# Kernel tuning notes

Measured on AMD Instinct MI355X. Metric: run time of the kernel, lower is better.

The kernel has to match this reference:

```python
import jax, jax.numpy as jnp
import numpy as np

CHANNELS = 8
IN_CHANNELS = 8
MASK_OUT_STRIDE = 4
WEIGHT_NUMS = [(IN_CHANNELS + 2) * CHANNELS, CHANNELS * CHANNELS, CHANNELS * 1]
BIAS_NUMS = [CHANNELS, CHANNELS, 1]
SOI = jnp.array([8.0, 16.0, 32.0, 64.0, 128.0], dtype=jnp.float32)
EPS = 1e-5


def compute_locations(h, w, stride):
    # (x, y) center of each stride-sized cell, row-major (y outer, x inner)
    sx = jnp.arange(w, dtype=jnp.float32) * stride + stride // 2
    sy = jnp.arange(h, dtype=jnp.float32) * stride + stride // 2
    yy, xx = jnp.meshgrid(sy, sx, indexing='ij')
    return jnp.stack([xx.reshape(-1), yy.reshape(-1)], axis=-1)  # [H*W, 2]


def aligned_bilinear(t, factor):
    # Matches AdelaiDet aligned_bilinear: replicate-pad right/bottom, bilinear
    # upsample align_corners=True to (f*h+1, f*w+1), replicate-pad top/left by
    # f//2, crop to (f*h, f*w).
    if factor == 1:
        return t
    n, c, h, w = t.shape
    t = jnp.pad(t, ((0, 0), (0, 0), (0, 1), (0, 1)), mode='edge')  # [n,c,h+1,w+1]
    oh, ow = factor * h + 1, factor * w + 1
    ys = jnp.arange(oh, dtype=jnp.float32) / factor  # align_corners mapping
    xs = jnp.arange(ow, dtype=jnp.float32) / factor
    y0 = jnp.floor(ys).astype(jnp.int32)
    x0 = jnp.floor(xs).astype(jnp.int32)
    y1 = jnp.minimum(y0 + 1, h)
    x1 = jnp.minimum(x0 + 1, w)
    wy = (ys - y0.astype(jnp.float32)).astype(t.dtype)
    wx = (xs - x0.astype(jnp.float32)).astype(t.dtype)
    ty = t[:, :, y0, :] * (1.0 - wy)[None, None, :, None] + t[:, :, y1, :] * wy[None, None, :, None]
    out = ty[:, :, :, x0] * (1.0 - wx) + ty[:, :, :, x1] * wx
    p = factor // 2
    out = jnp.pad(out, ((0, 0), (0, 0), (p, 0), (p, 0)), mode='edge')
    return out[:, :, :oh - 1, :ow - 1]


def parse_dynamic_params(params):
    n = params.shape[0]
    splits = jnp.split(params, np.cumsum(WEIGHT_NUMS + BIAS_NUMS)[:-1], axis=1)
    w0 = splits[0].reshape(n, CHANNELS, IN_CHANNELS + 2)
    w1 = splits[1].reshape(n, CHANNELS, CHANNELS)
    w2 = splits[2].reshape(n, 1, CHANNELS)
    b0 = splits[3].reshape(n, CHANNELS)
    b1 = splits[4].reshape(n, CHANNELS)
    b2 = splits[5].reshape(n, 1)
    return (w0, w1, w2), (b0, b1, b2)


def setup_inputs() -> dict:
    key = jax.random.key(0)
    ks = jax.random.split(key, 6)
    N, H, W = 2, 100, 136
    n_inst = 500
    return {
        'mask_feats': jax.random.normal(ks[0], (N, IN_CHANNELS, H, W), dtype=jnp.float32),
        'mask_head_params': jax.random.normal(ks[1], (n_inst, 169), dtype=jnp.float32),
        'locations_inst': jax.random.uniform(ks[2], (n_inst, 2), dtype=jnp.float32),
        'gt_bitmasks': jax.random.uniform(ks[3], (n_inst, 1, 2 * H, 2 * W), dtype=jnp.float32),
        'im_inds': jax.random.randint(ks[4], (n_inst,), 0, N, dtype=jnp.int64 if jax.config.jax_enable_x64 else jnp.int32),
        'fpn_levels': jax.random.randint(ks[5], (n_inst,), 0, 5, dtype=jnp.int64 if jax.config.jax_enable_x64 else jnp.int32),
        'mask_feat_stride': 8,
    }


def reference(mask_feats, mask_head_params, locations_inst, gt_bitmasks, im_inds, fpn_levels, mask_feat_stride):
    N, Cin, H, W = mask_feats.shape
    n = mask_head_params.shape[0]
    # relative coordinates, normalized by per-instance size-of-interest
    locs = compute_locations(H, W, mask_feat_stride)                 # [HW, 2]
    rel = locations_inst[:, None, :] - locs[None, :, :]              # [n, HW, 2]
    rel = jnp.transpose(rel, (0, 2, 1))                              # [n, 2, HW]
    soi = SOI[fpn_levels]                                            # [n]
    rel = (rel / soi[:, None, None]).astype(mask_feats.dtype)
    feats = mask_feats[im_inds].reshape(n, Cin, H * W)               # gather per instance
    x = jnp.concatenate([rel, feats], axis=1)                        # [n, Cin+2, HW]
    # per-instance 1x1 conv stack == batched small GEMMs
    (w0, w1, w2), (b0, b1, b2) = parse_dynamic_params(mask_head_params)
    x = jax.nn.relu(jnp.einsum('nci,nip->ncp', w0, x) + b0[:, :, None])
    x = jax.nn.relu(jnp.einsum('nci,nip->ncp', w1, x) + b1[:, :, None])
    x = jnp.einsum('nci,nip->ncp', w2, x) + b2[:, :, None]           # [n, 1, HW]
    logits = x.reshape(n, 1, H, W)
    logits = aligned_bilinear(logits, mask_feat_stride // MASK_OUT_STRIDE)
    scores = jax.nn.sigmoid(logits)                                  # [n, 1, 2H, 2W]
    # dice loss
    xs = scores.reshape(n, -1)
    t = gt_bitmasks.reshape(n, -1)
    inter = jnp.sum(xs * t, axis=1)
    union = jnp.sum(xs * xs, axis=1) + jnp.sum(t * t, axis=1) + EPS
    loss = 1.0 - 2.0 * inter / union
    return jnp.mean(loss)
```

## Files before the change

kernel.cpp:

```cpp
#include <hip/hip_runtime.h>
#include <hip/hip_bf16.h>
#include <math.h>

#define CIN      8
#define H_IN     100
#define W_IN     136
#define NPIX     (H_IN * W_IN)
#define OH       (2 * H_IN)
#define OW       (2 * W_IN)
#define ONPIX    (OH * OW)
#define NPARAMS  169
#define EPSV     1e-5f
#define NSLICE   4
#define KG4      34
#define KGROUPS  34
#define TASKS_B  (25 * KGROUPS)


__device__ __forceinline__ float sigmoidf_fast(float x) {
    float e = __expf(-x);
    return __builtin_amdgcn_rcpf(1.f + e);
}

__global__ __launch_bounds__(256, 4)
void mask_head_fused(const float* __restrict__ mask_feats,
                     const float* __restrict__ params,
                     const float* __restrict__ locs,
                     const float* __restrict__ gt,
                     const int*   __restrict__ im_inds,
                     const int*   __restrict__ fpn_levels,
                     float*       __restrict__ partials)
{
    const int inst  = blockIdx.x >> 2;
    const int slice = blockIdx.x & 3;
    const int tid   = threadIdx.x;

    const int r_start = (slice == 0) ? 0 : 25 * slice - 1;
    const int nrows   = (slice == 0) ? 25 : 26;
    const int ntask   = nrows * KG4;

    __shared__ float s_logit[26 * W_IN];
    __shared__ float s_red[12];

    const float* __restrict__ wp = params + (size_t)inst * NPARAMS;

    const int   im  = im_inds[inst];
    const int   lvl = fpn_levels[inst];
    const float inv_soi = exp2f(-(float)(3 + lvl));
    const float lx = locs[inst * 2 + 0];
    const float ly = locs[inst * 2 + 1];
    const float dx8 = 8.f * inv_soi;

    const float* feat = mask_feats + (size_t)im * (CIN * NPIX);
    const int goff = r_start * W_IN;

    #pragma unroll 1
    for (int it = 0; it < 4; ++it) {
        const int t = it * 256 + tid;
        const bool valid = t < ntask;
        const int tc = valid ? t : ntask - 1;
        const int r  = tc / KG4;
        const int k  = tc - r * KG4;
        const int lpx = r * W_IN + 4 * k;
        const float* fb = feat + (goff + lpx);

        float4 f[8];
        #pragma unroll
        for (int c = 0; c < CIN; ++c)
            f[c] = *(const float4*)(fb + c * NPIX);

        float in0[4];
        in0[0] = (lx - (float)(32 * k + 4)) * inv_soi;
        in0[1] = in0[0] - dx8;
        in0[2] = in0[1] - dx8;
        in0[3] = in0[2] - dx8;
        const float in1 = (ly - (float)((r_start + r) * 8 + 4)) * inv_soi;

        float o4[4];

#define DO_PX(J, COMP)                                                        \
        {                                                                     \
            float aj[8];                                                      \
            _Pragma("unroll")                                                 \
            for (int o = 0; o < 8; ++o)                                       \
                aj[o] = fmaf(wp[o * 10], in0[J],                              \
                             fmaf(wp[o * 10 + 1], in1, wp[152 + o]));         \
            _Pragma("unroll")                                                 \
            for (int c = 0; c < 8; ++c) {                                     \
                _Pragma("unroll")                                             \
                for (int o = 0; o < 8; ++o)                                   \
                    aj[o] = fmaf(wp[o * 10 + 2 + c], f[c].COMP, aj[o]);       \
            }                                                                 \
            _Pragma("unroll")                                                 \
            for (int o = 0; o < 8; ++o)                                       \
                aj[o] = fmaxf(aj[o], 0.f);                                    \
            float acc = wp[168];                                              \
            _Pragma("unroll")                                                 \
            for (int o = 0; o < 8; ++o) {                                     \
                float tt = wp[160 + o];                                       \
                _Pragma("unroll")                                             \
                for (int i = 0; i < 8; ++i)                                   \
                    tt = fmaf(wp[80 + o * 8 + i], aj[i], tt);                 \
                acc = fmaf(wp[144 + o], fmaxf(tt, 0.f), acc);                 \
            }                                                                 \
            o4[J] = acc;                                                      \
        }

        DO_PX(0, x)
        DO_PX(1, y)
        DO_PX(2, z)
        DO_PX(3, w)
#undef DO_PX

        if (valid) {
            float4 ov = {o4[0], o4[1], o4[2], o4[3]};
            *(float4*)(s_logit + lpx) = ov;
        }
    }

    __syncthreads();

    float inter = 0.f, ssum = 0.f, tsum = 0.f;
    const float* gtp = gt + (size_t)inst * ONPIX;
    const int pair_base = 25 * slice;

    #pragma unroll 1
    for (int base = 0; base < TASKS_B; base += 256) {
        const int task = base + tid;
        if (task < TASKS_B) {
            const int pl = task / KGROUPS;
            const int k  = task - pl * KGROUPS;
            const int pg = pair_base + pl;
            const int er = pg - r_start;
            const int pr = (pg > 0 ? pg - 1 : 0) - r_start;
            const float* E = s_logit + er * W_IN;
            const float* P = s_logit + pr * W_IN;
            const int c0  = 4 * k;
            const int cm1 = (k > 0) ? c0 - 1 : 0;

            const float* g0 = gtp + (size_t)(2 * pg) * OW + 8 * k;
            const float4 ga = *(const float4*)(g0);
            const float4 gb = *(const float4*)(g0 + 4);
            const float4 gc = *(const float4*)(g0 + OW);
            const float4 gd = *(const float4*)(g0 + OW + 4);
            const float4 e4 = *(const float4*)(E + c0);
            const float  em = E[cm1];
            const float4 p4 = *(const float4*)(P + c0);
            const float  pm = P[cm1];

            const float ecur[4] = {e4.x, e4.y, e4.z, e4.w};
            const float pcur[4] = {p4.x, p4.y, p4.z, p4.w};
            const float gav[8] = {ga.x, ga.y, ga.z, ga.w, gb.x, gb.y, gb.z, gb.w};
            const float gex[8] = {gc.x, gc.y, gc.z, gc.w, gd.x, gd.y, gd.z, gd.w};

            float Se_prev = em;
            float Sa_prev = 0.5f * (em + pm);
            #pragma unroll
            for (int j = 0; j < 4; ++j) {
                const float Se = ecur[j];
                const float Sa = 0.5f * (ecur[j] + pcur[j]);
                {
                    float s = sigmoidf_fast(0.5f * (Sa_prev + Sa));
                    float t2 = gav[2 * j];
                    inter = fmaf(s, t2, inter); ssum = fmaf(s, s, ssum); tsum = fmaf(t2, t2, tsum);
                    s = sigmoidf_fast(Sa);
                    t2 = gav[2 * j + 1];
                    inter = fmaf(s, t2, inter); ssum = fmaf(s, s, ssum); tsum = fmaf(t2, t2, tsum);
                }
                {
                    float s = sigmoidf_fast(0.5f * (Se_prev + Se));
                    float t2 = gex[2 * j];
                    inter = fmaf(s, t2, inter); ssum = fmaf(s, s, ssum); tsum = fmaf(t2, t2, tsum);
                    s = sigmoidf_fast(Se);
                    t2 = gex[2 * j + 1];
                    inter = fmaf(s, t2, inter); ssum = fmaf(s, s, ssum); tsum = fmaf(t2, t2, tsum);
                }
                Se_prev = Se;
                Sa_prev = Sa;
            }
        }
    }

    #pragma unroll
    for (int off = 32; off > 0; off >>= 1) {
        inter += __shfl_down(inter, off, 64);
        ssum  += __shfl_down(ssum,  off, 64);
        tsum  += __shfl_down(tsum,  off, 64);
    }
    const int wid = tid >> 6;
    if ((tid & 63) == 0) {
        s_red[wid * 3 + 0] = inter;
        s_red[wid * 3 + 1] = ssum;
        s_red[wid * 3 + 2] = tsum;
    }
    __syncthreads();
    if (tid == 0) {
        float I = 0.f, S = 0.f, T = 0.f;
        #pragma unroll
        for (int w = 0; w < 4; ++w) {
            I += s_red[w * 3 + 0];
            S += s_red[w * 3 + 1];
            T += s_red[w * 3 + 2];
        }
        partials[blockIdx.x * 3 + 0] = I;
        partials[blockIdx.x * 3 + 1] = S;
        partials[blockIdx.x * 3 + 2] = T;
    }
}

__global__ __launch_bounds__(512)
void loss_mean_kernel(const float* __restrict__ partials, float* __restrict__ out, int n)
{
    __shared__ float s_red[8];
    float v = 0.f;
    for (int i = threadIdx.x; i < n; i += 512) {
        float I = 0.f, S = 0.f, T = 0.f;
        #pragma unroll
        for (int s = 0; s < NSLICE; ++s) {
            const float* p = partials + (size_t)(i * NSLICE + s) * 3;
            I += p[0];
            S += p[1];
            T += p[2];
        }
        v += 1.f - 2.f * I / (S + T + EPSV);
    }
    #pragma unroll
    for (int off = 32; off > 0; off >>= 1) v += __shfl_down(v, off, 64);
    const int wid = threadIdx.x >> 6;
    if ((threadIdx.x & 63) == 0) s_red[wid] = v;
    __syncthreads();
    if (threadIdx.x == 0) {
        float s = 0.f;
        #pragma unroll
        for (int w = 0; w < 8; ++w) s += s_red[w];
        out[0] = s / (float)n;
    }
}

extern "C" void kernel_launch(void* const* d_in, const int* in_sizes, int n_in,
                              void* d_out, int out_size, void* d_ws, size_t ws_size,
                              hipStream_t stream)
{
    const float* mask_feats = (const float*)d_in[0];
    const float* params     = (const float*)d_in[1];
    const float* locs       = (const float*)d_in[2];
    const float* gt         = (const float*)d_in[3];
    const int*   im_inds    = (const int*)d_in[4];
    const int*   fpn_levels = (const int*)d_in[5];

    const int n = in_sizes[4];
    float* partials = (float*)d_ws;

    mask_head_fused<<<n * NSLICE, 256, 0, stream>>>(mask_feats, params, locs, gt,
                                                    im_inds, fpn_levels, partials);
    loss_mean_kernel<<<1, 512, 0, stream>>>(partials, (float*)d_out, n);
}
```

Before: 182.4 us.

## Prefetch first ground-truth rows into LDS asynchronously during conv phase

In the first iteration of the per-pixel conv loop, each block issues asynchronous global-to-LDS loads covering the first 11 row-pairs of its slice of the ground-truth mask. The later dice pass then reads those rows from LDS and fetches the rest from global memory as before. The aim is to hide part of the ground-truth fetch latency behind the conv arithmetic. The cost is about 24KB more LDS per block, which may lower occupancy, and the LDS prefetch is issued only by threads that have a valid conv task in the first iteration.

```diff
diff --git a/kernel.cpp b/kernel.cpp
--- a/kernel.cpp
+++ b/kernel.cpp
@@ -1,5 +1,4 @@
 #include <hip/hip_runtime.h>
-#include <hip/hip_bf16.h>
 #include <math.h>
 
 #define CIN      8
@@ -16,6 +15,13 @@
 #define KGROUPS  34
 #define TASKS_B  (25 * KGROUPS)
 
+#define GT_PRE_PAIRS 11
+#define GT_PRE_ROWS  (2 * GT_PRE_PAIRS)
+#define GT_PRE_F4    (GT_PRE_ROWS * OW / 4)
+
+#define GLOBAL_AS __attribute__((address_space(1)))
+#define LDS_AS    __attribute__((address_space(3)))
+
 
 __device__ __forceinline__ float sigmoidf_fast(float x) {
     float e = __expf(-x);
@@ -40,6 +46,7 @@
     const int ntask   = nrows * KG4;
 
     __shared__ float s_logit[26 * W_IN];
+    __shared__ float s_gt[GT_PRE_ROWS * OW];
     __shared__ float s_red[12];
 
     const float* __restrict__ wp = params + (size_t)inst * NPARAMS;
@@ -54,65 +61,80 @@
     const float* feat = mask_feats + (size_t)im * (CIN * NPIX);
     const int goff = r_start * W_IN;
 
+    const float* gtp  = gt + (size_t)inst * ONPIX;
+    const float* gpre = gtp + (size_t)(50 * slice) * OW;
+
     #pragma unroll 1
     for (int it = 0; it < 4; ++it) {
         const int t = it * 256 + tid;
-        const bool valid = t < ntask;
-        const int tc = valid ? t : ntask - 1;
-        const int r  = tc / KG4;
-        const int k  = tc - r * KG4;
-        const int lpx = r * W_IN + 4 * k;
-        const float* fb = feat + (goff + lpx);
-
-        float4 f[8];
-        #pragma unroll
-        for (int c = 0; c < CIN; ++c)
-            f[c] = *(const float4*)(fb + c * NPIX);
-
-        float in0[4];
-        in0[0] = (lx - (float)(32 * k + 4)) * inv_soi;
-        in0[1] = in0[0] - dx8;
-        in0[2] = in0[1] - dx8;
-        in0[3] = in0[2] - dx8;
-        const float in1 = (ly - (float)((r_start + r) * 8 + 4)) * inv_soi;
-
-        float o4[4];
+        if (t < ntask) {
+            const int r  = t / KG4;
+            const int k  = t - r * KG4;
+            const int lpx = r * W_IN + 4 * k;
+            const float* fb = feat + (goff + lpx);
+
+            float4 f[8];
+            #pragma unroll
+            for (int c = 0; c < CIN; ++c)
+                f[c] = *(const float4*)(fb + c * NPIX);
+
+            if (it == 0) {
+                #pragma unroll
+                for (int j = 0; j < 6; ++j) {
+                    const int fidx  = j * 256 + tid;
+                    const int wbase = j * 256 + (tid & ~63);
+                    if (fidx < GT_PRE_F4) {
+                        __builtin_amdgcn_global_load_lds(
+                            (const GLOBAL_AS void*)(gpre + (size_t)fidx * 4),
+                            (LDS_AS void*)(s_gt + (size_t)wbase * 4),
+                            16, 0, 0);
+                    }
+                }
+            }
+
+            float in0[4];
+            in0[0] = (lx - (float)(32 * k + 4)) * inv_soi;
+            in0[1] = in0[0] - dx8;
+            in0[2] = in0[1] - dx8;
+            in0[3] = in0[2] - dx8;
+            const float in1 = (ly - (float)((r_start + r) * 8 + 4)) * inv_soi;
+
+            float o4[4];
 
 #define DO_PX(J, COMP)                                                        \
-        {                                                                     \
-            float aj[8];                                                      \
-            _Pragma("unroll")                                                 \
-            for (int o = 0; o < 8; ++o)                                       \
-                aj[o] = fmaf(wp[o * 10], in0[J],                              \
-                             fmaf(wp[o * 10 + 1], in1, wp[152 + o]));         \
-            _Pragma("unroll")                                                 \
-            for (int c = 0; c < 8; ++c) {                                     \
+            {                                                                 \
+                float aj[8];                                                  \
                 _Pragma("unroll")                                             \
                 for (int o = 0; o < 8; ++o)                                   \
-                    aj[o] = fmaf(wp[o * 10 + 2 + c], f[c].COMP, aj[o]);       \
-            }                                                                 \
-            _Pragma("unroll")                                                 \
-            for (int o = 0; o < 8; ++o)                                       \
-                aj[o] = fmaxf(aj[o], 0.f);                                    \
-            float acc = wp[168];                                              \
-            _Pragma("unroll")                                                 \
-            for (int o = 0; o < 8; ++o) {                                     \
-                float tt = wp[160 + o];                                       \
-                _Pragma("unroll")                                             \
-                for (int i = 0; i < 8; ++i)                                   \
-                    tt = fmaf(wp[80 + o * 8 + i], aj[i], tt);                 \
-                acc = fmaf(wp[144 + o], fmaxf(tt, 0.f), acc);                 \
-            }                                                                 \
-            o4[J] = acc;                                                      \
-        }
-
-        DO_PX(0, x)
-        DO_PX(1, y)
-        DO_PX(2, z)
-        DO_PX(3, w)
+                    aj[o] = fmaf(wp[o * 10], in0[J],                          \
+                                 fmaf(wp[o * 10 + 1], in1, wp[152 + o]));     \
+                _Pragma("unroll")                                             \
+                for (int c = 0; c < 8; ++c) {                                 \
+                    _Pragma("unroll")                                         \
+                    for (int o = 0; o < 8; ++o)                               \
+                        aj[o] = fmaf(wp[o * 10 + 2 + c], f[c].COMP, aj[o]);   \
+                }                                                             \
+                _Pragma("unroll")                                             \
+                for (int o = 0; o < 8; ++o)                                   \
+                    aj[o] = fmaxf(aj[o], 0.f);                                \
+                float acc = wp[168];                                          \
+                _Pragma("unroll")                                             \
+                for (int o = 0; o < 8; ++o) {                                 \
+                    float tt = wp[160 + o];                                   \
+                    _Pragma("unroll")                                         \
+                    for (int i = 0; i < 8; ++i)                               \
+                        tt = fmaf(wp[80 + o * 8 + i], aj[i], tt);             \
+                    acc = fmaf(wp[144 + o], fmaxf(tt, 0.f), acc);             \
+                }                                                             \
+                o4[J] = acc;                                                  \
+            }
+
+            DO_PX(0, x)
+            DO_PX(1, y)
+            DO_PX(2, z)
+            DO_PX(3, w)
 #undef DO_PX
 
-        if (valid) {
             float4 ov = {o4[0], o4[1], o4[2], o4[3]};
             *(float4*)(s_logit + lpx) = ov;
         }
@@ -121,7 +143,6 @@
     __syncthreads();
 
     float inter = 0.f, ssum = 0.f, tsum = 0.f;
-    const float* gtp = gt + (size_t)inst * ONPIX;
     const int pair_base = 25 * slice;
 
     #pragma unroll 1
@@ -138,11 +159,20 @@
             const int c0  = 4 * k;
             const int cm1 = (k > 0) ? c0 - 1 : 0;
 
-            const float* g0 = gtp + (size_t)(2 * pg) * OW + 8 * k;
-            const float4 ga = *(const float4*)(g0);
-            const float4 gb = *(const float4*)(g0 + 4);
-            const float4 gc = *(const float4*)(g0 + OW);
-            const float4 gd = *(const float4*)(g0 + OW + 4);
+            float4 ga, gb, gc, gd;
+            if (pl < GT_PRE_PAIRS) {
+                const float* l0 = s_gt + (size_t)(2 * pl) * OW + 8 * k;
+                ga = *(const float4*)(l0);
+                gb = *(const float4*)(l0 + 4);
+                gc = *(const float4*)(l0 + OW);
+                gd = *(const float4*)(l0 + OW + 4);
+            } else {
+                const float* g0 = gtp + (size_t)(2 * pg) * OW + 8 * k;
+                ga = *(const float4*)(g0);
+                gb = *(const float4*)(g0 + 4);
+                gc = *(const float4*)(g0 + OW);
+                gd = *(const float4*)(g0 + OW + 4);
+            }
             const float4 e4 = *(const float4*)(E + c0);
             const float  em = E[cm1];
             const float4 p4 = *(const float4*)(P + c0);
```

Result: slower. 193.2 us (+5.9%).

## Software-pipeline feature and GT loads with double buffers, halve per-thread pixel width

Applied to the files above, without the earlier changes.

Stage A now handles 2 pixels per task instead of 4 and uses two float2 register buffers, so the next task's feature loads are issued before the current task's MLP is computed. Stage B prefetches the first ground-truth tile before the barrier and then alternates two float4 buffers, so later GT loads overlap the sigmoid and dice work. This is meant to hide global-memory latency behind arithmetic, at the cost of more live registers and more, narrower loads. The per-pixel row-coordinate term is also hoisted out of the pixel loop.

```diff
diff --git a/kernel.cpp b/kernel.cpp
--- a/kernel.cpp
+++ b/kernel.cpp
@@ -1,5 +1,4 @@
 #include <hip/hip_runtime.h>
-#include <hip/hip_bf16.h>
 #include <math.h>
 
 #define CIN      8
@@ -12,7 +11,7 @@
 #define NPARAMS  169
 #define EPSV     1e-5f
 #define NSLICE   4
-#define KG4      34
+#define KG2      68
 #define KGROUPS  34
 #define TASKS_B  (25 * KGROUPS)
 
@@ -37,7 +36,7 @@
 
     const int r_start = (slice == 0) ? 0 : 25 * slice - 1;
     const int nrows   = (slice == 0) ? 25 : 26;
-    const int ntask   = nrows * KG4;
+    const int ntask   = nrows * KG2;
 
     __shared__ float s_logit[26 * W_IN];
     __shared__ float s_red[12];
@@ -54,37 +53,35 @@
     const float* feat = mask_feats + (size_t)im * (CIN * NPIX);
     const int goff = r_start * W_IN;
 
-    #pragma unroll 1
-    for (int it = 0; it < 4; ++it) {
-        const int t = it * 256 + tid;
-        const bool valid = t < ntask;
-        const int tc = valid ? t : ntask - 1;
-        const int r  = tc / KG4;
-        const int k  = tc - r * KG4;
-        const int lpx = r * W_IN + 4 * k;
-        const float* fb = feat + (goff + lpx);
-
-        float4 f[8];
+    auto loadf = [&](float2 (&f)[8], int t) {
+        const int r  = t / KG2;
+        const int k  = t - r * KG2;
+        const float* fb = feat + (goff + r * W_IN + 2 * k);
         #pragma unroll
         for (int c = 0; c < CIN; ++c)
-            f[c] = *(const float4*)(fb + c * NPIX);
-
-        float in0[4];
-        in0[0] = (lx - (float)(32 * k + 4)) * inv_soi;
+            f[c] = *(const float2*)(fb + c * NPIX);
+    };
+
+    auto computeA = [&](const float2 (&f)[8], int t) {
+        const int r   = t / KG2;
+        const int k   = t - r * KG2;
+        const int lpx = r * W_IN + 2 * k;
+        float in0[2];
+        in0[0] = (lx - (float)(16 * k + 4)) * inv_soi;
         in0[1] = in0[0] - dx8;
-        in0[2] = in0[1] - dx8;
-        in0[3] = in0[2] - dx8;
         const float in1 = (ly - (float)((r_start + r) * 8 + 4)) * inv_soi;
-
-        float o4[4];
-
-#define DO_PX(J, COMP)                                                        \
+        float basev[8];
+        #pragma unroll
+        for (int o = 0; o < 8; ++o)
+            basev[o] = fmaf(wp[o * 10 + 1], in1, wp[152 + o]);
+
+        float o2[2];
+#define DO_PX2(J, COMP)                                                       \
         {                                                                     \
             float aj[8];                                                      \
             _Pragma("unroll")                                                 \
             for (int o = 0; o < 8; ++o)                                       \
-                aj[o] = fmaf(wp[o * 10], in0[J],                              \
-                             fmaf(wp[o * 10 + 1], in1, wp[152 + o]));         \
+                aj[o] = fmaf(wp[o * 10], in0[J], basev[o]);                    \
             _Pragma("unroll")                                                 \
             for (int c = 0; c < 8; ++c) {                                     \
                 _Pragma("unroll")                                             \
@@ -103,82 +100,113 @@
                     tt = fmaf(wp[80 + o * 8 + i], aj[i], tt);                 \
                 acc = fmaf(wp[144 + o], fmaxf(tt, 0.f), acc);                 \
             }                                                                 \
-            o4[J] = acc;                                                      \
-        }
-
-        DO_PX(0, x)
-        DO_PX(1, y)
-        DO_PX(2, z)
-        DO_PX(3, w)
-#undef DO_PX
-
-        if (valid) {
-            float4 ov = {o4[0], o4[1], o4[2], o4[3]};
-            *(float4*)(s_logit + lpx) = ov;
-        }
-    }
-
-    __syncthreads();
+            o2[J] = acc;                                                      \
+        }
+        DO_PX2(0, x)
+        DO_PX2(1, y)
+#undef DO_PX2
+        float2 ov = {o2[0], o2[1]};
+        *(float2*)(s_logit + lpx) = ov;
+    };
+
+    {
+        float2 fA[8], fB[8];
+        int t0 = tid;
+        loadf(fA, t0);
+        #pragma unroll 1
+        for (int it = 0; it < 4; ++it) {
+            const int t1 = t0 + 256;
+            if (t1 < ntask) loadf(fB, t1);
+            if (t0 < ntask) computeA(fA, t0);
+            const int t2 = t0 + 512;
+            if (t2 < ntask) loadf(fA, t2);
+            if (t1 < ntask) computeA(fB, t1);
+            t0 = t2;
+        }
+    }
 
     float inter = 0.f, ssum = 0.f, tsum = 0.f;
     const float* gtp = gt + (size_t)inst * ONPIX;
     const int pair_base = 25 * slice;
 
-    #pragma unroll 1
-    for (int base = 0; base < TASKS_B; base += 256) {
-        const int task = base + tid;
-        if (task < TASKS_B) {
-            const int pl = task / KGROUPS;
-            const int k  = task - pl * KGROUPS;
-            const int pg = pair_base + pl;
-            const int er = pg - r_start;
-            const int pr = (pg > 0 ? pg - 1 : 0) - r_start;
-            const float* E = s_logit + er * W_IN;
-            const float* P = s_logit + pr * W_IN;
-            const int c0  = 4 * k;
-            const int cm1 = (k > 0) ? c0 - 1 : 0;
-
-            const float* g0 = gtp + (size_t)(2 * pg) * OW + 8 * k;
-            const float4 ga = *(const float4*)(g0);
-            const float4 gb = *(const float4*)(g0 + 4);
-            const float4 gc = *(const float4*)(g0 + OW);
-            const float4 gd = *(const float4*)(g0 + OW + 4);
-            const float4 e4 = *(const float4*)(E + c0);
-            const float  em = E[cm1];
-            const float4 p4 = *(const float4*)(P + c0);
-            const float  pm = P[cm1];
-
-            const float ecur[4] = {e4.x, e4.y, e4.z, e4.w};
-            const float pcur[4] = {p4.x, p4.y, p4.z, p4.w};
-            const float gav[8] = {ga.x, ga.y, ga.z, ga.w, gb.x, gb.y, gb.z, gb.w};
-            const float gex[8] = {gc.x, gc.y, gc.z, gc.w, gd.x, gd.y, gd.z, gd.w};
-
-            float Se_prev = em;
-            float Sa_prev = 0.5f * (em + pm);
-            #pragma unroll
-            for (int j = 0; j < 4; ++j) {
-                const float Se = ecur[j];
-                const float Sa = 0.5f * (ecur[j] + pcur[j]);
-                {
-                    float s = sigmoidf_fast(0.5f * (Sa_prev + Sa));
-                    float t2 = gav[2 * j];
-                    inter = fmaf(s, t2, inter); ssum = fmaf(s, s, ssum); tsum = fmaf(t2, t2, tsum);
-                    s = sigmoidf_fast(Sa);
-                    t2 = gav[2 * j + 1];
-                    inter = fmaf(s, t2, inter); ssum = fmaf(s, s, ssum); tsum = fmaf(t2, t2, tsum);
-                }
-                {
-                    float s = sigmoidf_fast(0.5f * (Se_prev + Se));
-                    float t2 = gex[2 * j];
-                    inter = fmaf(s, t2, inter); ssum = fmaf(s, s, ssum); tsum = fmaf(t2, t2, tsum);
-                    s = sigmoidf_fast(Se);
-                    t2 = gex[2 * j + 1];
-                    inter = fmaf(s, t2, inter); ssum = fmaf(s, s, ssum); tsum = fmaf(t2, t2, tsum);
-                }
-                Se_prev = Se;
-                Sa_prev = Sa;
+    auto loadgt = [&](float4 (&g)[4], int task) {
+        const int pl = task / KGROUPS;
+        const int k  = task - pl * KGROUPS;
+        const int pg = pair_base + pl;
+        const float* g0 = gtp + (size_t)(2 * pg) * OW + 8 * k;
+        g[0] = *(const float4*)(g0);
+        g[1] = *(const float4*)(g0 + 4);
+        g[2] = *(const float4*)(g0 + OW);
+        g[3] = *(const float4*)(g0 + OW + 4);
+    };
+
+    auto computeB = [&](const float4 (&g)[4], int task) {
+        const int pl = task / KGROUPS;
+        const int k  = task - pl * KGROUPS;
+        const int pg = pair_base + pl;
+        const int er = pg - r_start;
+        const int pr = (pg > 0 ? pg - 1 : 0) - r_start;
+        const float* E = s_logit + er * W_IN;
+        const float* P = s_logit + pr * W_IN;
+        const int c0  = 4 * k;
+        const int cm1 = (k > 0) ? c0 - 1 : 0;
+
+        const float4 e4 = *(const float4*)(E + c0);
+        const float  em = E[cm1];
+        const float4 p4 = *(const float4*)(P + c0);
+        const float  pm = P[cm1];
+
+        const float ecur[4] = {e4.x, e4.y, e4.z, e4.w};
+        const float pcur[4] = {p4.x, p4.y, p4.z, p4.w};
+        const float gav[8] = {g[0].x, g[0].y, g[0].z, g[0].w,
+                              g[1].x, g[1].y, g[1].z, g[1].w};
+        const float gex[8] = {g[2].x, g[2].y, g[2].z, g[2].w,
+                              g[3].x, g[3].y, g[3].z, g[3].w};
+
+        float Se_prev = em;
+        float Sa_prev = 0.5f * (em + pm);
+        #pragma unroll
+        for (int j = 0; j < 4; ++j) {
+            const float Se = ecur[j];
+            const float Sa = 0.5f * (ecur[j] + pcur[j]);
+            {
+                float s = sigmoidf_fast(0.5f * (Sa_prev + Sa));
+                float t2 = gav[2 * j];
+                inter = fmaf(s, t2, inter); ssum = fmaf(s, s, ssum); tsum = fmaf(t2, t2, tsum);
+                s = sigmoidf_fast(Sa);
+                t2 = gav[2 * j + 1];
+                inter = fmaf(s, t2, inter); ssum = fmaf(s, s, ssum); tsum = fmaf(t2, t2, tsum);
             }
-        }
+            {
+                float s = sigmoidf_fast(0.5f * (Se_prev + Se));
+                float t2 = gex[2 * j];
+                inter = fmaf(s, t2, inter); ssum = fmaf(s, s, ssum); tsum = fmaf(t2, t2, tsum);
+                s = sigmoidf_fast(Se);
+                t2 = gex[2 * j + 1];
+                inter = fmaf(s, t2, inter); ssum = fmaf(s, s, ssum); tsum = fmaf(t2, t2, tsum);
+            }
+            Se_prev = Se;
+            Sa_prev = Sa;
+        }
+    };
+
+    {
+        float4 gA[4], gB[4];
+        const int t0 = tid;
+        loadgt(gA, t0);
+
+        __syncthreads();
+
+        const int t1 = t0 + 256;
+        const int t2 = t0 + 512;
+        const int t3 = t0 + 768;
+        if (t1 < TASKS_B) loadgt(gB, t1);
+        computeB(gA, t0);
+        if (t2 < TASKS_B) loadgt(gA, t2);
+        if (t1 < TASKS_B) computeB(gB, t1);
+        if (t3 < TASKS_B) loadgt(gB, t3);
+        if (t2 < TASKS_B) computeB(gA, t2);
+        if (t3 < TASKS_B) computeB(gB, t3);
     }
 
     #pragma unroll
```

Measured after the change: 186.7 us. 1.02x slower.
